# Optimization experiments

Hardware: AMD Instinct MI355X
Metric: run time of the kernel (lower is better)

## Reference

```python
import jax, jax.numpy as jnp
import numpy as np
import math

EMBED_DIM = 768
NUM_HEADS = 12


def setup_inputs() -> dict:
    key = jax.random.key(0)
    ks = jax.random.split(key, 5)
    R, C, B, E = 128, 256, 1, EMBED_DIM
    s = 1.0 / math.sqrt(E)
    x = jax.random.normal(ks[0], (R, C, B, E), dtype=jnp.float32)
    wq = jax.random.normal(ks[1], (E, E), dtype=jnp.float32) * s
    wk = jax.random.normal(ks[2], (E, E), dtype=jnp.float32) * s
    wv = jax.random.normal(ks[3], (E, E), dtype=jnp.float32) * s
    wo = jax.random.normal(ks[4], (E, E), dtype=jnp.float32) * s
    z = jnp.zeros((E,), dtype=jnp.float32)
    return {"x": x, "wq": wq, "bq": z, "wk": wk, "bk": z,
            "wv": wv, "bv": z, "wo": wo, "bo": z}


def reference(x, wq, bq, wk, bk, wv, bv, wo, bo):
    R, C, B, E = x.shape
    H = NUM_HEADS
    D = E // H
    shape = (R, C, B, H, D)
    # tied row attention scaling: 1/sqrt(head_dim) * 1/sqrt(num_rows)
    scaling = (D ** -0.5) / math.sqrt(R)
    q = jnp.reshape(x @ wq + bq, shape) * scaling
    k = jnp.reshape(x @ wk + bk, shape)
    v = jnp.reshape(x @ wv + bv, shape)
    # logits summed (tied) over the row axis r: [H, B, C, C]
    attn_weights = jnp.einsum('rinhd,rjnhd->hnij', q, k)
    attn_probs = jax.nn.softmax(attn_weights, axis=-1)
    # broadcast probs back to every row
    context = jnp.einsum('hnij,rjnhd->rinhd', attn_probs, v)
    context = jnp.reshape(context, (R, C, B, E))
    return context @ wo + bo
```

## Files before the change

kernel.cpp:

```cpp
#include <hip/hip_runtime.h>
#include <hip/hip_bf16.h>
#include <math.h>

typedef __bf16 bf16_t;
typedef __bf16 vbf4 __attribute__((ext_vector_type(4)));
typedef __bf16 vbf8 __attribute__((ext_vector_type(8)));
typedef float  vf4  __attribute__((ext_vector_type(4)));

#define OFF_XB   0ull
#define OFF_Q    50331648ull
#define OFF_K    100663296ull
#define OFF_VT   150994944ull
#define OFF_L    201326592ull
#define OFF_P    204472320ull
#define OFF_WQ   206045184ull
#define OFF_WK   207224832ull
#define OFF_WV   208404480ull
#define OFF_WO   209584128ull

__device__ __forceinline__ void stage_tile128x64(const bf16_t* __restrict__ g,
                                                 int ld, int row0, int k0,
                                                 bf16_t* lds, int tid) {
  const int wave = tid >> 6;
  const int lane = tid & 63;
  const int js = (lane & 7) ^ (lane >> 3);
#pragma unroll
  for (int cc = 0; cc < 4; ++cc) {
    const int chunk = cc * 4 + wave;
    const int row = chunk * 8 + (lane >> 3);
    const bf16_t* gp = g + (size_t)(row0 + row) * ld + k0 + js * 8;
    bf16_t* lp = lds + chunk * 512 + lane * 8;
    __builtin_amdgcn_global_load_lds(
        (const __attribute__((address_space(1))) void*)gp,
        (__attribute__((address_space(3))) void*)lp, 16, 0, 0);
  }
}

__device__ __forceinline__ vbf8 lds_frag(const bf16_t* s, int rr, int ko) {
  const int c = (ko >> 3) ^ (rr & 7);
  return *(const vbf8*)&s[rr * 64 + (c << 3)];
}

__device__ __forceinline__ void gemm_mainloop(const bf16_t* __restrict__ A, int lda, int m0,
                                              const bf16_t* __restrict__ Bt, int ldb, int n0,
                                              int kbeg, int kend,
                                              bf16_t* As, bf16_t* Bs,
                                              vf4 (&acc)[4][4]) {
  const int tid = threadIdx.x;
  const int lane = tid & 63;
  const int wave = tid >> 6;
  const int wm0 = (wave >> 1) * 64;
  const int wn0 = (wave & 1) * 64;
  const int fm = lane & 15;
  const int fk = (lane >> 4) * 8;

  for (int k0 = kbeg; k0 < kend; k0 += 64) {
    stage_tile128x64(A, lda, m0, k0, As, tid);
    stage_tile128x64(Bt, ldb, n0, k0, Bs, tid);
    __syncthreads();
#pragma unroll
    for (int kk = 0; kk < 64; kk += 32) {
      vbf8 af[4], bfv[4];
#pragma unroll
      for (int mt = 0; mt < 4; ++mt)
        af[mt] = lds_frag(As, wm0 + mt * 16 + fm, kk + fk);
#pragma unroll
      for (int nt = 0; nt < 4; ++nt)
        bfv[nt] = lds_frag(Bs, wn0 + nt * 16 + fm, kk + fk);
#pragma unroll
      for (int mt = 0; mt < 4; ++mt)
#pragma unroll
        for (int nt = 0; nt < 4; ++nt)
          acc[mt][nt] = __builtin_amdgcn_mfma_f32_16x16x32_bf16(af[mt], bfv[nt],
                                                                acc[mt][nt], 0, 0, 0);
    }
    __syncthreads();
  }
}

__device__ __forceinline__ void zero_acc(vf4 (&acc)[4][4]) {
  const vf4 z = {0.f, 0.f, 0.f, 0.f};
#pragma unroll
  for (int mt = 0; mt < 4; ++mt)
#pragma unroll
    for (int nt = 0; nt < 4; ++nt) acc[mt][nt] = z;
}

__global__ __launch_bounds__(256) void pack_x(const float* __restrict__ x,
                                              bf16_t* __restrict__ Xb) {
  const size_t idx = (size_t)blockIdx.x * 256 + threadIdx.x;
  const float4 v = ((const float4*)x)[idx];
  vbf4 o;
  o[0] = (bf16_t)v.x; o[1] = (bf16_t)v.y; o[2] = (bf16_t)v.z; o[3] = (bf16_t)v.w;
  ((vbf4*)Xb)[idx] = o;
}

__global__ __launch_bounds__(256) void pack_w(const float* __restrict__ wq,
                                              const float* __restrict__ wk,
                                              const float* __restrict__ wv,
                                              const float* __restrict__ wo,
                                              bf16_t* __restrict__ Wq, bf16_t* __restrict__ Wk,
                                              bf16_t* __restrict__ Wv, bf16_t* __restrict__ Wo,
                                              float scaling) {
  const int idx = blockIdx.x * 256 + threadIdx.x;
  const int wid = blockIdx.y;
  const float* src = (wid == 0) ? wq : (wid == 1) ? wk : (wid == 2) ? wv : wo;
  bf16_t* dst = (wid == 0) ? Wq : (wid == 1) ? Wk : (wid == 2) ? Wv : Wo;
  const int n = idx / 768;
  const int k = idx - n * 768;
  float v = src[k * 768 + n];
  if (wid == 0) v *= scaling;
  dst[idx] = (bf16_t)v;
}

__global__ __launch_bounds__(256) void qkv_gemm(const bf16_t* __restrict__ Xb,
                                                const bf16_t* __restrict__ Wq,
                                                const bf16_t* __restrict__ Wk,
                                                const bf16_t* __restrict__ Wv,
                                                const float* __restrict__ bq,
                                                const float* __restrict__ bk,
                                                const float* __restrict__ bv,
                                                bf16_t* __restrict__ Qh,
                                                bf16_t* __restrict__ Kh,
                                                bf16_t* __restrict__ Vt,
                                                float scaling) {
  __shared__ __align__(16) bf16_t As[128 * 64];
  __shared__ __align__(16) bf16_t Bs[128 * 64];
  const int bx = blockIdx.x;
  const int m_idx = bx / 18;
  const int rem = bx - m_idx * 18;
  const int n_idx = rem / 3;
  const int z = rem - n_idx * 3;
  const int m0 = m_idx * 128;
  const int n0 = n_idx * 128;
  const bf16_t* W = (z == 0) ? Wq : (z == 1) ? Wk : Wv;
  vf4 acc[4][4];
  zero_acc(acc);
  gemm_mainloop(Xb, 768, m0, W, 768, n0, 0, 768, As, Bs, acc);

  const int lane = threadIdx.x & 63;
  const int wave = threadIdx.x >> 6;
  const int wm0 = (wave >> 1) * 64;
  const int wn0 = (wave & 1) * 64;
  const int col = lane & 15;
  const int rq = (lane >> 4) * 4;
  const float* bias = (z == 0) ? bq : (z == 1) ? bk : bv;
  const float bsc = (z == 0) ? scaling : 1.0f;

  if (z < 2) {
    bf16_t* O = (z == 0) ? Qh : Kh;
#pragma unroll
    for (int mt = 0; mt < 4; ++mt) {
#pragma unroll
      for (int nt = 0; nt < 4; ++nt) {
        const int n = n0 + wn0 + nt * 16 + col;
        const int h = n >> 6, d = n & 63;
        const float bb = bias[n] * bsc;
#pragma unroll
        for (int i = 0; i < 4; ++i) {
          const int m = m0 + wm0 + mt * 16 + rq + i;
          const int r = m >> 8, c = m & 255;
          O[(size_t)(h * 256 + c) * 8192 + (r << 6) + d] = (bf16_t)(acc[mt][nt][i] + bb);
        }
      }
    }
  } else {
#pragma unroll
    for (int mt = 0; mt < 4; ++mt) {
      const int mb = m0 + wm0 + mt * 16 + rq;
      const int r = mb >> 8, c = mb & 255;
#pragma unroll
      for (int nt = 0; nt < 4; ++nt) {
        const int n = n0 + wn0 + nt * 16 + col;
        const int h = n >> 6, d = n & 63;
        const float bb = bias[n];
        vbf4 pk;
#pragma unroll
        for (int i = 0; i < 4; ++i) pk[i] = (bf16_t)(acc[mt][nt][i] + bb);
        *(vbf4*)&Vt[(size_t)h * 2097152 + ((size_t)((r << 6) + d)) * 256 + c] = pk;
      }
    }
  }
}

__global__ __launch_bounds__(256) void logits_gemm(const bf16_t* __restrict__ Qh,
                                                   const bf16_t* __restrict__ Kh,
                                                   float* __restrict__ L) {
  __shared__ __align__(16) bf16_t As[128 * 64];
  __shared__ __align__(16) bf16_t Bs[128 * 64];
  const int n0 = blockIdx.x * 128;
  const int m0 = blockIdx.y * 128;
  const int h = blockIdx.z >> 3;
  const int kseg = blockIdx.z & 7;
  const bf16_t* A = Qh + (size_t)h * (256 * 8192);
  const bf16_t* B = Kh + (size_t)h * (256 * 8192);
  vf4 acc[4][4];
  zero_acc(acc);
  gemm_mainloop(A, 8192, m0, B, 8192, n0, kseg * 1024, kseg * 1024 + 1024, As, Bs, acc);

  const int lane = threadIdx.x & 63;
  const int wave = threadIdx.x >> 6;
  const int wm0 = (wave >> 1) * 64;
  const int wn0 = (wave & 1) * 64;
  const int col = lane & 15;
  const int rq = (lane >> 4) * 4;
  float* Lh = L + (size_t)h * 65536;
#pragma unroll
  for (int mt = 0; mt < 4; ++mt)
#pragma unroll
    for (int nt = 0; nt < 4; ++nt) {
      const int n = n0 + wn0 + nt * 16 + col;
#pragma unroll
      for (int i = 0; i < 4; ++i) {
        const int m = m0 + wm0 + mt * 16 + rq + i;
        atomicAdd(&Lh[(size_t)m * 256 + n], acc[mt][nt][i]);
      }
    }
}

__global__ __launch_bounds__(256) void softmax_k(const float* __restrict__ L,
                                                 bf16_t* __restrict__ P) {
  const int row = blockIdx.x * 4 + (threadIdx.x >> 6);
  const int lane = threadIdx.x & 63;
  const float4 v4 = ((const float4*)(L + (size_t)row * 256))[lane];
  float a = v4.x, b = v4.y, c = v4.z, d = v4.w;
  float mx = fmaxf(fmaxf(a, b), fmaxf(c, d));
#pragma unroll
  for (int off = 32; off; off >>= 1) mx = fmaxf(mx, __shfl_xor(mx, off));
  a = expf(a - mx); b = expf(b - mx); c = expf(c - mx); d = expf(d - mx);
  float s = a + b + c + d;
#pragma unroll
  for (int off = 32; off; off >>= 1) s += __shfl_xor(s, off);
  const float inv = 1.0f / s;
  vbf4 o;
  o[0] = (bf16_t)(a * inv); o[1] = (bf16_t)(b * inv);
  o[2] = (bf16_t)(c * inv); o[3] = (bf16_t)(d * inv);
  ((vbf4*)(P + (size_t)row * 256))[lane] = o;
}

__global__ __launch_bounds__(256) void ctx_gemm(const bf16_t* __restrict__ P,
                                                const bf16_t* __restrict__ Vt,
                                                bf16_t* __restrict__ CtxTok) {
  __shared__ __align__(16) bf16_t As[128 * 64];
  __shared__ __align__(16) bf16_t Bs[128 * 64];
  const int m0 = blockIdx.x * 128;
  const int n0 = blockIdx.y * 128;
  const int h = blockIdx.z;
  const bf16_t* A = P + (size_t)h * 65536;
  const bf16_t* B = Vt + (size_t)h * 2097152;
  vf4 acc[4][4];
  zero_acc(acc);
  gemm_mainloop(A, 256, m0, B, 256, n0, 0, 256, As, Bs, acc);

  const int lane = threadIdx.x & 63;
  const int wave = threadIdx.x >> 6;
  const int wm0 = (wave >> 1) * 64;
  const int wn0 = (wave & 1) * 64;
  const int col = lane & 15;
  const int rq = (lane >> 4) * 4;
#pragma unroll
  for (int mt = 0; mt < 4; ++mt)
#pragma unroll
    for (int nt = 0; nt < 4; ++nt) {
      const int n = n0 + wn0 + nt * 16 + col;
      const int r = n >> 6, d = n & 63;
#pragma unroll
      for (int i = 0; i < 4; ++i) {
        const int m = m0 + wm0 + mt * 16 + rq + i;
        CtxTok[(size_t)((r << 8) + m) * 768 + (h << 6) + d] = (bf16_t)acc[mt][nt][i];
      }
    }
}

__global__ __launch_bounds__(256) void out_gemm(const bf16_t* __restrict__ Ctx,
                                                const bf16_t* __restrict__ Wo,
                                                const float* __restrict__ bo,
                                                float* __restrict__ Out) {
  __shared__ __align__(16) bf16_t As[128 * 64];
  __shared__ __align__(16) bf16_t Bs[128 * 64];
  const int bx = blockIdx.x;
  const int m_idx = bx / 6;
  const int n_idx = bx - m_idx * 6;
  const int m0 = m_idx * 128;
  const int n0 = n_idx * 128;
  vf4 acc[4][4];
  zero_acc(acc);
  gemm_mainloop(Ctx, 768, m0, Wo, 768, n0, 0, 768, As, Bs, acc);

  const int lane = threadIdx.x & 63;
  const int wave = threadIdx.x >> 6;
  const int wm0 = (wave >> 1) * 64;
  const int wn0 = (wave & 1) * 64;
  const int col = lane & 15;
  const int rq = (lane >> 4) * 4;
#pragma unroll
  for (int mt = 0; mt < 4; ++mt)
#pragma unroll
    for (int nt = 0; nt < 4; ++nt) {
      const int n = n0 + wn0 + nt * 16 + col;
      const float bb = bo[n];
#pragma unroll
      for (int i = 0; i < 4; ++i) {
        const int m = m0 + wm0 + mt * 16 + rq + i;
        Out[(size_t)m * 768 + n] = acc[mt][nt][i] + bb;
      }
    }
}

extern "C" void kernel_launch(void* const* d_in, const int* in_sizes, int n_in,
                              void* d_out, int out_size, void* d_ws, size_t ws_size,
                              hipStream_t stream) {
  const float* x  = (const float*)d_in[0];
  const float* wq = (const float*)d_in[1];
  const float* bq = (const float*)d_in[2];
  const float* wk = (const float*)d_in[3];
  const float* bk = (const float*)d_in[4];
  const float* wv = (const float*)d_in[5];
  const float* bv = (const float*)d_in[6];
  const float* wo = (const float*)d_in[7];
  const float* bo = (const float*)d_in[8];
  float* out = (float*)d_out;

  char* ws = (char*)d_ws;
  bf16_t* Xb  = (bf16_t*)(ws + OFF_XB);
  bf16_t* Ctx = (bf16_t*)(ws + OFF_XB);
  bf16_t* Qh  = (bf16_t*)(ws + OFF_Q);
  bf16_t* Kh  = (bf16_t*)(ws + OFF_K);
  bf16_t* Vt  = (bf16_t*)(ws + OFF_VT);
  float*  L   = (float*)(ws + OFF_L);
  bf16_t* P   = (bf16_t*)(ws + OFF_P);
  bf16_t* Wq  = (bf16_t*)(ws + OFF_WQ);
  bf16_t* Wk  = (bf16_t*)(ws + OFF_WK);
  bf16_t* Wv  = (bf16_t*)(ws + OFF_WV);
  bf16_t* Wo  = (bf16_t*)(ws + OFF_WO);

  const float scaling = 0.125f / sqrtf(128.0f);

  hipMemsetAsync(L, 0, (size_t)12 * 256 * 256 * 4, stream);
  pack_x<<<24576, 256, 0, stream>>>(x, Xb);
  pack_w<<<dim3(2304, 4), 256, 0, stream>>>(wq, wk, wv, wo, Wq, Wk, Wv, Wo, scaling);
  qkv_gemm<<<4608, 256, 0, stream>>>(Xb, Wq, Wk, Wv, bq, bk, bv, Qh, Kh, Vt, scaling);
  logits_gemm<<<dim3(2, 2, 96), 256, 0, stream>>>(Qh, Kh, L);
  softmax_k<<<768, 256, 0, stream>>>(L, P);
  ctx_gemm<<<dim3(2, 64, 12), 256, 0, stream>>>(P, Vt, Ctx);
  out_gemm<<<1536, 256, 0, stream>>>(Ctx, Wo, bo, out);

  (void)in_sizes; (void)n_in; (void)out_size; (void)ws_size;
}
```

Before: 498.7 us.

## Use 256x128 GEMM tiles, split-K partials instead of atomics, tiled weight transpose

```diff
diff --git a/kernel.cpp b/kernel.cpp
--- a/kernel.cpp
+++ b/kernel.cpp
@@ -11,21 +11,21 @@
 #define OFF_Q    50331648ull
 #define OFF_K    100663296ull
 #define OFF_VT   150994944ull
-#define OFF_L    201326592ull
-#define OFF_P    204472320ull
-#define OFF_WQ   206045184ull
-#define OFF_WK   207224832ull
-#define OFF_WV   208404480ull
-#define OFF_WO   209584128ull
-
-__device__ __forceinline__ void stage_tile128x64(const bf16_t* __restrict__ g,
-                                                 int ld, int row0, int k0,
-                                                 bf16_t* lds, int tid) {
+#define OFF_P    201326592ull
+#define OFF_WQ   202899456ull
+#define OFF_WK   204079104ull
+#define OFF_WV   205258752ull
+#define OFF_WO   206438400ull
+
+template <int ROWS>
+__device__ __forceinline__ void stage_tile(const bf16_t* __restrict__ g,
+                                           int ld, int row0, int k0,
+                                           bf16_t* lds, int tid) {
   const int wave = tid >> 6;
   const int lane = tid & 63;
   const int js = (lane & 7) ^ (lane >> 3);
 #pragma unroll
-  for (int cc = 0; cc < 4; ++cc) {
+  for (int cc = 0; cc < ROWS / 32; ++cc) {
     const int chunk = cc * 4 + wave;
     const int row = chunk * 8 + (lane >> 3);
     const bf16_t* gp = g + (size_t)(row0 + row) * ld + k0 + js * 8;
@@ -41,11 +41,11 @@
   return *(const vbf8*)&s[rr * 64 + (c << 3)];
 }
 
-__device__ __forceinline__ void gemm_mainloop(const bf16_t* __restrict__ A, int lda, int m0,
-                                              const bf16_t* __restrict__ Bt, int ldb, int n0,
-                                              int kbeg, int kend,
-                                              bf16_t* As, bf16_t* Bs,
-                                              vf4 (&acc)[4][4]) {
+__device__ __forceinline__ void gemm_mainloop128(const bf16_t* __restrict__ A, int lda, int m0,
+                                                 const bf16_t* __restrict__ Bt, int ldb, int n0,
+                                                 int kbeg, int kend,
+                                                 bf16_t* As, bf16_t* Bs,
+                                                 vf4 (&acc)[4][4]) {
   const int tid = threadIdx.x;
   const int lane = tid & 63;
   const int wave = tid >> 6;
@@ -53,20 +53,17 @@
   const int wn0 = (wave & 1) * 64;
   const int fm = lane & 15;
   const int fk = (lane >> 4) * 8;
-
   for (int k0 = kbeg; k0 < kend; k0 += 64) {
-    stage_tile128x64(A, lda, m0, k0, As, tid);
-    stage_tile128x64(Bt, ldb, n0, k0, Bs, tid);
+    stage_tile<128>(A, lda, m0, k0, As, tid);
+    stage_tile<128>(Bt, ldb, n0, k0, Bs, tid);
     __syncthreads();
 #pragma unroll
     for (int kk = 0; kk < 64; kk += 32) {
       vbf8 af[4], bfv[4];
 #pragma unroll
-      for (int mt = 0; mt < 4; ++mt)
-        af[mt] = lds_frag(As, wm0 + mt * 16 + fm, kk + fk);
-#pragma unroll
-      for (int nt = 0; nt < 4; ++nt)
-        bfv[nt] = lds_frag(Bs, wn0 + nt * 16 + fm, kk + fk);
+      for (int mt = 0; mt < 4; ++mt) af[mt] = lds_frag(As, wm0 + mt * 16 + fm, kk + fk);
+#pragma unroll
+      for (int nt = 0; nt < 4; ++nt) bfv[nt] = lds_frag(Bs, wn0 + nt * 16 + fm, kk + fk);
 #pragma unroll
       for (int mt = 0; mt < 4; ++mt)
 #pragma unroll
@@ -78,10 +75,54 @@
   }
 }
 
-__device__ __forceinline__ void zero_acc(vf4 (&acc)[4][4]) {
+__device__ __forceinline__ void gemm_mainloop256(const bf16_t* __restrict__ A, int lda, int m0,
+                                                 const bf16_t* __restrict__ Bt, int ldb, int n0,
+                                                 int kbeg, int kend,
+                                                 bf16_t* As, bf16_t* Bs,
+                                                 vf4 (&acc)[8][4]) {
+  const int tid = threadIdx.x;
+  const int lane = tid & 63;
+  const int wave = tid >> 6;
+  const int wq0 = (wave >> 1) * 64;
+  const int wn0 = (wave & 1) * 64;
+  const int fm = lane & 15;
+  const int fk = (lane >> 4) * 8;
+  for (int k0 = kbeg; k0 < kend; k0 += 64) {
+    stage_tile<256>(A, lda, m0, k0, As, tid);
+    stage_tile<128>(Bt, ldb, n0, k0, Bs, tid);
+    __syncthreads();
+#pragma unroll
+    for (int kk = 0; kk < 64; kk += 32) {
+      vbf8 af[8], bfv[4];
+#pragma unroll
+      for (int mt = 0; mt < 8; ++mt) {
+        const int rr = ((mt & 4) << 5) + wq0 + (mt & 3) * 16 + fm;
+        af[mt] = lds_frag(As, rr, kk + fk);
+      }
+#pragma unroll
+      for (int nt = 0; nt < 4; ++nt) bfv[nt] = lds_frag(Bs, wn0 + nt * 16 + fm, kk + fk);
+#pragma unroll
+      for (int mt = 0; mt < 8; ++mt)
+#pragma unroll
+        for (int nt = 0; nt < 4; ++nt)
+          acc[mt][nt] = __builtin_amdgcn_mfma_f32_16x16x32_bf16(af[mt], bfv[nt],
+                                                                acc[mt][nt], 0, 0, 0);
+    }
+    __syncthreads();
+  }
+}
+
+__device__ __forceinline__ void zero_acc4(vf4 (&acc)[4][4]) {
   const vf4 z = {0.f, 0.f, 0.f, 0.f};
 #pragma unroll
   for (int mt = 0; mt < 4; ++mt)
+#pragma unroll
+    for (int nt = 0; nt < 4; ++nt) acc[mt][nt] = z;
+}
+__device__ __forceinline__ void zero_acc8(vf4 (&acc)[8][4]) {
+  const vf4 z = {0.f, 0.f, 0.f, 0.f};
+#pragma unroll
+  for (int mt = 0; mt < 8; ++mt)
 #pragma unroll
     for (int nt = 0; nt < 4; ++nt) acc[mt][nt] = z;
 }
@@ -102,45 +143,56 @@
                                               bf16_t* __restrict__ Wq, bf16_t* __restrict__ Wk,
                                               bf16_t* __restrict__ Wv, bf16_t* __restrict__ Wo,
                                               float scaling) {
-  const int idx = blockIdx.x * 256 + threadIdx.x;
+  __shared__ float t[64][65];
   const int wid = blockIdx.y;
   const float* src = (wid == 0) ? wq : (wid == 1) ? wk : (wid == 2) ? wv : wo;
   bf16_t* dst = (wid == 0) ? Wq : (wid == 1) ? Wk : (wid == 2) ? Wv : Wo;
-  const int n = idx / 768;
-  const int k = idx - n * 768;
-  float v = src[k * 768 + n];
-  if (wid == 0) v *= scaling;
-  dst[idx] = (bf16_t)v;
-}
-
-__global__ __launch_bounds__(256) void qkv_gemm(const bf16_t* __restrict__ Xb,
-                                                const bf16_t* __restrict__ Wq,
-                                                const bf16_t* __restrict__ Wk,
-                                                const bf16_t* __restrict__ Wv,
-                                                const float* __restrict__ bq,
-                                                const float* __restrict__ bk,
-                                                const float* __restrict__ bv,
-                                                bf16_t* __restrict__ Qh,
-                                                bf16_t* __restrict__ Kh,
-                                                bf16_t* __restrict__ Vt,
-                                                float scaling) {
-  __shared__ __align__(16) bf16_t As[128 * 64];
+  const float sc = (wid == 0) ? scaling : 1.0f;
+  const int kt = (blockIdx.x / 12) * 64;
+  const int nt = (blockIdx.x % 12) * 64;
+  const int tx = threadIdx.x & 63;
+  const int ty = threadIdx.x >> 6;
+#pragma unroll
+  for (int p = 0; p < 16; ++p) {
+    const int k = ty + p * 4;
+    t[tx][k] = src[(size_t)(kt + k) * 768 + nt + tx] * sc;
+  }
+  __syncthreads();
+#pragma unroll
+  for (int p = 0; p < 16; ++p) {
+    const int n = ty + p * 4;
+    dst[(size_t)(nt + n) * 768 + kt + tx] = (bf16_t)t[n][tx];
+  }
+}
+
+__global__ __launch_bounds__(256, 2) void qkv_gemm(const bf16_t* __restrict__ Xb,
+                                                   const bf16_t* __restrict__ Wq,
+                                                   const bf16_t* __restrict__ Wk,
+                                                   const bf16_t* __restrict__ Wv,
+                                                   const float* __restrict__ bq,
+                                                   const float* __restrict__ bk,
+                                                   const float* __restrict__ bv,
+                                                   bf16_t* __restrict__ Qh,
+                                                   bf16_t* __restrict__ Kh,
+                                                   bf16_t* __restrict__ Vt,
+                                                   float scaling) {
+  __shared__ __align__(16) bf16_t As[256 * 64];
   __shared__ __align__(16) bf16_t Bs[128 * 64];
   const int bx = blockIdx.x;
   const int m_idx = bx / 18;
   const int rem = bx - m_idx * 18;
   const int n_idx = rem / 3;
   const int z = rem - n_idx * 3;
-  const int m0 = m_idx * 128;
+  const int m0 = m_idx * 256;
   const int n0 = n_idx * 128;
   const bf16_t* W = (z == 0) ? Wq : (z == 1) ? Wk : Wv;
-  vf4 acc[4][4];
-  zero_acc(acc);
-  gemm_mainloop(Xb, 768, m0, W, 768, n0, 0, 768, As, Bs, acc);
+  vf4 acc[8][4];
+  zero_acc8(acc);
+  gemm_mainloop256(Xb, 768, m0, W, 768, n0, 0, 768, As, Bs, acc);
 
   const int lane = threadIdx.x & 63;
   const int wave = threadIdx.x >> 6;
-  const int wm0 = (wave >> 1) * 64;
+  const int wq0 = (wave >> 1) * 64;
   const int wn0 = (wave & 1) * 64;
   const int col = lane & 15;
   const int rq = (lane >> 4) * 4;
@@ -150,7 +202,7 @@
   if (z < 2) {
     bf16_t* O = (z == 0) ? Qh : Kh;
 #pragma unroll
-    for (int mt = 0; mt < 4; ++mt) {
+    for (int mt = 0; mt < 8; ++mt) {
 #pragma unroll
       for (int nt = 0; nt < 4; ++nt) {
         const int n = n0 + wn0 + nt * 16 + col;
@@ -158,7 +210,7 @@
         const float bb = bias[n] * bsc;
 #pragma unroll
         for (int i = 0; i < 4; ++i) {
-          const int m = m0 + wm0 + mt * 16 + rq + i;
+          const int m = m0 + ((mt & 4) << 5) + wq0 + (mt & 3) * 16 + rq + i;
           const int r = m >> 8, c = m & 255;
           O[(size_t)(h * 256 + c) * 8192 + (r << 6) + d] = (bf16_t)(acc[mt][nt][i] + bb);
         }
@@ -166,8 +218,8 @@
     }
   } else {
 #pragma unroll
-    for (int mt = 0; mt < 4; ++mt) {
-      const int mb = m0 + wm0 + mt * 16 + rq;
+    for (int mt = 0; mt < 8; ++mt) {
+      const int mb = m0 + ((mt & 4) << 5) + wq0 + (mt & 3) * 16 + rq;
       const int r = mb >> 8, c = mb & 255;
 #pragma unroll
       for (int nt = 0; nt < 4; ++nt) {
@@ -185,18 +237,18 @@
 
 __global__ __launch_bounds__(256) void logits_gemm(const bf16_t* __restrict__ Qh,
                                                    const bf16_t* __restrict__ Kh,
-                                                   float* __restrict__ L) {
+                                                   float* __restrict__ Lp) {
   __shared__ __align__(16) bf16_t As[128 * 64];
   __shared__ __align__(16) bf16_t Bs[128 * 64];
   const int n0 = blockIdx.x * 128;
   const int m0 = blockIdx.y * 128;
-  const int h = blockIdx.z >> 3;
-  const int kseg = blockIdx.z & 7;
+  const int h = blockIdx.z >> 4;
+  const int kseg = blockIdx.z & 15;
   const bf16_t* A = Qh + (size_t)h * (256 * 8192);
   const bf16_t* B = Kh + (size_t)h * (256 * 8192);
   vf4 acc[4][4];
-  zero_acc(acc);
-  gemm_mainloop(A, 8192, m0, B, 8192, n0, kseg * 1024, kseg * 1024 + 1024, As, Bs, acc);
+  zero_acc4(acc);
+  gemm_mainloop128(A, 8192, m0, B, 8192, n0, kseg * 512, kseg * 512 + 512, As, Bs, acc);
 
   const int lane = threadIdx.x & 63;
   const int wave = threadIdx.x >> 6;
@@ -204,7 +256,7 @@
   const int wn0 = (wave & 1) * 64;
   const int col = lane & 15;
   const int rq = (lane >> 4) * 4;
-  float* Lh = L + (size_t)h * 65536;
+  float* Lph = Lp + ((size_t)(kseg * 12 + h)) * 65536;
 #pragma unroll
   for (int mt = 0; mt < 4; ++mt)
 #pragma unroll
@@ -213,17 +265,21 @@
 #pragma unroll
       for (int i = 0; i < 4; ++i) {
         const int m = m0 + wm0 + mt * 16 + rq + i;
-        atomicAdd(&Lh[(size_t)m * 256 + n], acc[mt][nt][i]);
-      }
-    }
-}
-
-__global__ __launch_bounds__(256) void softmax_k(const float* __restrict__ L,
+        Lph[(size_t)m * 256 + n] = acc[mt][nt][i];
+      }
+    }
+}
+
+__global__ __launch_bounds__(256) void softmax_k(const float* __restrict__ Lp,
                                                  bf16_t* __restrict__ P) {
   const int row = blockIdx.x * 4 + (threadIdx.x >> 6);
   const int lane = threadIdx.x & 63;
-  const float4 v4 = ((const float4*)(L + (size_t)row * 256))[lane];
-  float a = v4.x, b = v4.y, c = v4.z, d = v4.w;
+  float a = 0.f, b = 0.f, c = 0.f, d = 0.f;
+#pragma unroll
+  for (int ks = 0; ks < 16; ++ks) {
+    const float4 v4 = ((const float4*)(Lp + (size_t)ks * 786432 + (size_t)row * 256))[lane];
+    a += v4.x; b += v4.y; c += v4.z; d += v4.w;
+  }
   float mx = fmaxf(fmaxf(a, b), fmaxf(c, d));
 #pragma unroll
   for (int off = 32; off; off >>= 1) mx = fmaxf(mx, __shfl_xor(mx, off));
@@ -238,70 +294,69 @@
   ((vbf4*)(P + (size_t)row * 256))[lane] = o;
 }
 
-__global__ __launch_bounds__(256) void ctx_gemm(const bf16_t* __restrict__ P,
-                                                const bf16_t* __restrict__ Vt,
-                                                bf16_t* __restrict__ CtxTok) {
-  __shared__ __align__(16) bf16_t As[128 * 64];
+__global__ __launch_bounds__(256, 2) void ctx_gemm(const bf16_t* __restrict__ P,
+                                                   const bf16_t* __restrict__ Vt,
+                                                   bf16_t* __restrict__ CtxTok) {
+  __shared__ __align__(16) bf16_t As[256 * 64];
   __shared__ __align__(16) bf16_t Bs[128 * 64];
-  const int m0 = blockIdx.x * 128;
-  const int n0 = blockIdx.y * 128;
-  const int h = blockIdx.z;
+  const int n0 = blockIdx.x * 128;
+  const int h = blockIdx.y;
   const bf16_t* A = P + (size_t)h * 65536;
   const bf16_t* B = Vt + (size_t)h * 2097152;
-  vf4 acc[4][4];
-  zero_acc(acc);
-  gemm_mainloop(A, 256, m0, B, 256, n0, 0, 256, As, Bs, acc);
+  vf4 acc[8][4];
+  zero_acc8(acc);
+  gemm_mainloop256(A, 256, 0, B, 256, n0, 0, 256, As, Bs, acc);
 
   const int lane = threadIdx.x & 63;
   const int wave = threadIdx.x >> 6;
-  const int wm0 = (wave >> 1) * 64;
+  const int wq0 = (wave >> 1) * 64;
   const int wn0 = (wave & 1) * 64;
   const int col = lane & 15;
   const int rq = (lane >> 4) * 4;
 #pragma unroll
-  for (int mt = 0; mt < 4; ++mt)
+  for (int mt = 0; mt < 8; ++mt)
 #pragma unroll
     for (int nt = 0; nt < 4; ++nt) {
       const int n = n0 + wn0 + nt * 16 + col;
       const int r = n >> 6, d = n & 63;
 #pragma unroll
       for (int i = 0; i < 4; ++i) {
-        const int m = m0 + wm0 + mt * 16 + rq + i;
+        const int m = ((mt & 4) << 5) + wq0 + (mt & 3) * 16 + rq + i;
         CtxTok[(size_t)((r << 8) + m) * 768 + (h << 6) + d] = (bf16_t)acc[mt][nt][i];
       }
     }
 }
 
-__global__ __launch_bounds__(256) void out_gemm(const bf16_t* __restrict__ Ctx,
-                                                const bf16_t* __restrict__ Wo,
-                                                const float* __restrict__ bo,
-                                                float* __restrict__ Out) {
-  __shared__ __align__(16) bf16_t As[128 * 64];
+__global__ __launch_bounds__(256, 2) void out_gemm(const bf16_t* __restrict__ Ctx,
+                                                   const bf16_t* __restrict__ Wo,
+                                                   const float* __restrict__ bo,
+                                                   float* __restrict__ Out) {
+  __shared__ __align__(16) bf16_t As[256 * 64];
   __shared__ __align__(16) bf16_t Bs[128 * 64];
   const int bx = blockIdx.x;
   const int m_idx = bx / 6;
   const int n_idx = bx - m_idx * 6;
-  const int m0 = m_idx * 128;
+  const int m0 = m_idx * 256;
   const int n0 = n_idx * 128;
-  vf4 acc[4][4];
-  zero_acc(acc);
-  gemm_mainloop(Ctx, 768, m0, Wo, 768, n0, 0, 768, As, Bs, acc);
+  vf4 acc[8][4];
+  zero_acc8(acc);
+  gemm_mainloop256(Ctx, 768, m0, Wo, 768, n0, 0, 768, As, Bs, acc);
 
   const int lane = threadIdx.x & 63;
   const int wave = threadIdx.x >> 6;
-  const int wm0 = (wave >> 1) * 64;
+  const int wq0 = (wave >> 1) * 64;
   const int wn0 = (wave & 1) * 64;
   const int col = lane & 15;
   const int rq = (lane >> 4) * 4;
 #pragma unroll
-  for (int mt = 0; mt < 4; ++mt)
+  for (int mt = 0; mt < 8; ++mt)
 #pragma unroll
     for (int nt = 0; nt < 4; ++nt) {
       const int n = n0 + wn0 + nt * 16 + col;
       const float bb = bo[n];
 #pragma unroll
       for (int i = 0; i < 4; ++i) {
-        const int m = m0 + wm0 + mt * 16 + rq + i;
+        const int m = m0 + ((mt & 4) << 5) + wq0 + (mt & 3) * 16 + rq + i;
         Out[(size_t)m * 768 + n] = acc[mt][nt][i] + bb;
       }
     }
@@ -323,11 +378,11 @@
 
   char* ws = (char*)d_ws;
   bf16_t* Xb  = (bf16_t*)(ws + OFF_XB);
+  float*  Lp  = (float*)(ws + OFF_XB);
   bf16_t* Ctx = (bf16_t*)(ws + OFF_XB);
   bf16_t* Qh  = (bf16_t*)(ws + OFF_Q);
   bf16_t* Kh  = (bf16_t*)(ws + OFF_K);
   bf16_t* Vt  = (bf16_t*)(ws + OFF_VT);
-  float*  L   = (float*)(ws + OFF_L);
   bf16_t* P   = (bf16_t*)(ws + OFF_P);
   bf16_t* Wq  = (bf16_t*)(ws + OFF_WQ);
   bf16_t* Wk  = (bf16_t*)(ws + OFF_WK);
@@ -336,14 +391,13 @@
 
   const float scaling = 0.125f / sqrtf(128.0f);
 
-  hipMemsetAsync(L, 0, (size_t)12 * 256 * 256 * 4, stream);
   pack_x<<<24576, 256, 0, stream>>>(x, Xb);
-  pack_w<<<dim3(2304, 4), 256, 0, stream>>>(wq, wk, wv, wo, Wq, Wk, Wv, Wo, scaling);
-  qkv_gemm<<<4608, 256, 0, stream>>>(Xb, Wq, Wk, Wv, bq, bk, bv, Qh, Kh, Vt, scaling);
-  logits_gemm<<<dim3(2, 2, 96), 256, 0, stream>>>(Qh, Kh, L);
-  softmax_k<<<768, 256, 0, stream>>>(L, P);
-  ctx_gemm<<<dim3(2, 64, 12), 256, 0, stream>>>(P, Vt, Ctx);
-  out_gemm<<<1536, 256, 0, stream>>>(Ctx, Wo, bo, out);
+  pack_w<<<dim3(144, 4), 256, 0, stream>>>(wq, wk, wv, wo, Wq, Wk, Wv, Wo, scaling);
+  qkv_gemm<<<2304, 256, 0, stream>>>(Xb, Wq, Wk, Wv, bq, bk, bv, Qh, Kh, Vt, scaling);
+  logits_gemm<<<dim3(2, 2, 192), 256, 0, stream>>>(Qh, Kh, Lp);
+  softmax_k<<<768, 256, 0, stream>>>(Lp, P);
+  ctx_gemm<<<dim3(64, 12), 256, 0, stream>>>(P, Vt, Ctx);
+  out_gemm<<<768, 256, 0, stream>>>(Ctx, Wo, bo, out);
 
   (void)in_sizes; (void)n_in; (void)out_size; (void)ws_size;
 }
```

New measurement: 455.4 us. 1.1x faster.
